# Kernel tuning notes

Measured on AMD Instinct MI355X. Metric: run time of the kernel, lower is better.

Reference implementation:

```python
import jax, jax.numpy as jnp
import numpy as np

N = 100000          # nodes
E = 1600000         # edges (avg degree 16)
D = 128             # prototype feature dim
C = 100             # num classes
NUM_LAYERS = 3      # propagation layers


def setup_inputs() -> dict:
    key = jax.random.key(0)
    k1, k2, k3, k4 = jax.random.split(key, 4)
    train_mask = jax.random.randint(k1, (N,), 0, 2) > 0                # bool [N]
    labels_all = jax.random.randint(k2, (N,), 0, C)                    # int   [N]
    edge_index = jax.random.randint(k3, (2, E), 0, N)                  # int   [2,E]
    global_protos = jax.random.normal(k4, (C, D), dtype=jnp.float32)   # [C,D]
    alpha = jnp.float32(0.5)                                           # learnable scalar
    return dict(train_mask=train_mask, global_protos=global_protos,
                labels_all=labels_all, edge_index=edge_index, alpha=alpha)


def _label_propagate(y0, edge_index, alpha):
    # symmetric GCN normalization D^-1/2 A D^-1/2 (no self loops), as in PyG LabelPropagation
    src, dst = edge_index[0], edge_index[1]
    deg = jax.ops.segment_sum(jnp.ones((E,), y0.dtype), dst, num_segments=N)
    deg_inv_sqrt = jnp.where(deg > 0, jax.lax.rsqrt(jnp.maximum(deg, 1.0)), 0.0)
    norm = deg_inv_sqrt[src] * deg_inv_sqrt[dst]                       # [E]
    res = (1.0 - alpha) * y0                                           # residual term
    out = y0
    for _ in range(NUM_LAYERS):
        msgs = out[src] * norm[:, None]                                # gather [E,D]
        agg = jax.ops.segment_sum(msgs, dst, num_segments=N)           # scatter-add [N,D]
        out = jnp.clip(alpha * agg + res, 0.0, 1.0)                    # post_step clamp
    return out


def reference(train_mask, global_protos, labels_all, edge_index, alpha):
    # proto_rep[train_mask] = global_protos[labels_all[train_mask]], zeros elsewhere
    y0 = jnp.where(train_mask[:, None], global_protos[labels_all], 0.0)  # [N,D]
    return _label_propagate(y0, edge_index, alpha)
```

## Files before the change

### kernel.cpp

```cpp
#include <hip/hip_runtime.h>
#include <stdint.h>

typedef _Float16 f16;

#define N_NODES 100000
#define N_EDGES 1600000
#define CAP     64
#define NC      196
#define SLOTS   40
#define SEGCAP  12288
#define EPB     4096
#define SPAD    (CAP + 4)


__global__ __launch_bounds__(256) void bin_kernel(
    const int* __restrict__ src, const int* __restrict__ dst,
    int* __restrict__ gcur, unsigned int* __restrict__ gbins) {
    __shared__ int lcnt[NC];
    __shared__ int gb[NC];
    __shared__ unsigned int lbuf[NC * SLOTS];
    int t = threadIdx.x;
    for (int b = t; b < NC; b += 256) lcnt[b] = 0;
    __syncthreads();

    int base = blockIdx.x * EPB;
    int sv[16], dv[16];
#pragma unroll
    for (int k = 0; k < 16; ++k) {
        int i = base + k * 256 + t;
        sv[k] = (i < N_EDGES) ? src[i] : -1;
        dv[k] = (i < N_EDGES) ? dst[i] : 0;
    }
#pragma unroll
    for (int k = 0; k < 16; ++k) {
        if (sv[k] >= 0) {
            int d = dv[k];
            int cb = d >> 9;
            unsigned rec = (unsigned)sv[k] | ((unsigned)(d & 511) << 17);
            int pos = atomicAdd(&lcnt[cb], 1);
            if (pos < SLOTS) {
                lbuf[cb * SLOTS + pos] = rec;
            } else {
                int gp = atomicAdd(&gcur[cb], 1);
                if (gp < SEGCAP) gbins[(size_t)cb * SEGCAP + gp] = rec;
            }
        }
    }
    __syncthreads();
    if (t < NC) {
        int c = lcnt[t]; if (c > SLOTS) c = SLOTS;
        gb[t] = atomicAdd(&gcur[t], c);
    }
    __syncthreads();
    int wave = t >> 6, lane = t & 63;
    for (int b = wave; b < NC; b += 4) {
        int c = lcnt[b]; if (c > SLOTS) c = SLOTS;
        if (lane < c)
            gbins[(size_t)b * SEGCAP + gb[b] + lane] = lbuf[b * SLOTS + lane];
    }
}


__global__ __launch_bounds__(512) void csr_kernel(
    const unsigned int* __restrict__ gbins, const int* __restrict__ gcur,
    int* __restrict__ cnt, int* __restrict__ csr, float* __restrict__ dis,
    const int* __restrict__ mask, const int* __restrict__ labels,
    int* __restrict__ c0, int2* __restrict__ meta,
    const float* __restrict__ protos, f16* __restrict__ pf16) {
    __shared__ int lc[128];
    __shared__ int rows[128][CAP];
    int cb = blockIdx.x >> 2;
    int sb = blockIdx.x & 3;
    int t = threadIdx.x;
    if (t < 128) lc[t] = 0;
    __syncthreads();
    int m = gcur[cb]; if (m > SEGCAP) m = SEGCAP;
    const unsigned int* seg = gbins + (size_t)cb * SEGCAP;
    int base = (cb << 9) + (sb << 7);
    for (int i = t; i < m; i += 512) {
        unsigned v = seg[i];
        int dl = (int)(v >> 17);
        if ((dl >> 7) == sb) {
            int local = dl & 127;
            int pos = atomicAdd(&lc[local], 1);
            if (pos < CAP) rows[local][pos] = (int)(v & 0x1FFFF);
        }
    }
    __syncthreads();
    if (t < 128) {
        int n = base + t;
        if (n < N_NODES) {
            int d = lc[t];
            cnt[n] = d;
            float dv = (d > 0) ? rsqrtf((float)d) : 0.0f;
            dis[n] = dv;
            int c = mask[n] ? labels[n] : -1;
            c0[n] = c;
            meta[n] = make_int2(__float_as_int(dv), c);
        }
    }
    uint4* csr4 = (uint4*)csr;
    for (int idx = t; idx < 128 * 16; idx += 512) {
        int node = idx >> 4, ch = idx & 15;
        int n = base + node;
        if (n < N_NODES) {
            int d = lc[node]; if (d > CAP) d = CAP;
            if (ch * 4 < d) {
                uint4 w;
                w.x = (unsigned)rows[node][ch * 4 + 0];
                w.y = (unsigned)rows[node][ch * 4 + 1];
                w.z = (unsigned)rows[node][ch * 4 + 2];
                w.w = (unsigned)rows[node][ch * 4 + 3];
                csr4[(size_t)n * 16 + ch] = w;
            }
        }
    }
    if (blockIdx.x < 25) pf16[blockIdx.x * 512 + t] = (f16)protos[blockIdx.x * 512 + t];
}


__global__ __launch_bounds__(256) void prop0_kernel(
    const f16* __restrict__ pf16, uint8_t* __restrict__ out,
    const int* __restrict__ cnt, const int* __restrict__ csr,
    const float* __restrict__ dis, const int* __restrict__ c0,
    const int2* __restrict__ meta, int2* __restrict__ csr2,
    const float* __restrict__ protos, const float* __restrict__ alpha_p) {
    __shared__ uint2 smeta[4][4][SPAD];
    int t = threadIdx.x;
    int wave = t >> 6, lane = t & 63;
    int grp = lane >> 4, s16 = lane & 15;
    int n = blockIdx.x * 16 + wave * 4 + grp;

    float alpha = *alpha_p;
    int m = cnt[n]; if (m > CAP) m = CAP;
    float dn = dis[n];
    const int* bucket = csr + (size_t)n * CAP;
    int2* bucket2 = csr2 + (size_t)n * CAP;

    int mm = m;
    { int o = __shfl_xor(mm, 16); mm = mm > o ? mm : o;
      o = __shfl_xor(mm, 32);     mm = mm > o ? mm : o; }
    int mp = (mm + 3) & ~3;

    for (int e = s16; e < mp; e += 16) {
        unsigned wb = 0, off = 0;
        if (e < m) {
            int s = bucket[e];
            int2 mt = meta[s];
            float wpre = __int_as_float(mt.x) * dn;
            bucket2[e] = make_int2(s, __float_as_int(wpre));
            int c = mt.y;
            if (c >= 0) { wb = __float_as_uint(wpre); off = (unsigned)c << 4; }
        }
        smeta[wave][grp][e] = make_uint2(wb, off);
    }

    const uint4* md = (const uint4*)&smeta[wave][grp][0];
    const uint4* r4 = (const uint4*)pf16;
    float acc[8] = {0.f, 0.f, 0.f, 0.f, 0.f, 0.f, 0.f, 0.f};

    uint4 mA0, mA1, gA0, gA1, gA2, gA3;
    uint4 mB0, mB1, gB0, gB1, gB2, gB3;
#define LOADB(MM0, MM1, G0, G1, G2, G3, J) do {            \
    MM0 = md[(J) >> 1]; MM1 = md[((J) >> 1) + 1];          \
    G0 = r4[MM0.y + s16]; G1 = r4[MM0.w + s16];            \
    G2 = r4[MM1.y + s16]; G3 = r4[MM1.w + s16]; } while (0)
#define COMP1(WB, G) do {                                  \
    union { uint4 u; f16 h[8]; } q_; q_.u = (G);           \
    float w_ = __uint_as_float(WB);                        \
    _Pragma("unroll")                                      \
    for (int i_ = 0; i_ < 8; ++i_)                         \
        acc[i_] = fmaf((float)q_.h[i_], w_, acc[i_]); } while (0)
#define COMP(MM0, MM1, G0, G1, G2, G3) do {                \
    COMP1(MM0.x, G0); COMP1(MM0.z, G1);                    \
    COMP1(MM1.x, G2); COMP1(MM1.z, G3); } while (0)
    if (mp > 0) {
        LOADB(mA0, mA1, gA0, gA1, gA2, gA3, 0);
        for (int j = 0; j < mp; j += 8) {
            if (j + 4 < mp) LOADB(mB0, mB1, gB0, gB1, gB2, gB3, j + 4);
            COMP(mA0, mA1, gA0, gA1, gA2, gA3);
            if (j + 8 < mp) LOADB(mA0, mA1, gA0, gA1, gA2, gA3, j + 8);
            if (j + 4 < mp) COMP(mB0, mB1, gB0, gB1, gB2, gB3);
        }
    }
#undef LOADB
#undef COMP1
#undef COMP

    int cn = c0[n];
    float ra = 1.f - alpha;
    float y[8] = {0.f, 0.f, 0.f, 0.f, 0.f, 0.f, 0.f, 0.f};
    if (cn >= 0) {
        const float4* pr = (const float4*)(protos + (size_t)cn * 128) + (s16 << 1);
        float4 p0 = pr[0], p1 = pr[1];
        y[0] = p0.x; y[1] = p0.y; y[2] = p0.z; y[3] = p0.w;
        y[4] = p1.x; y[5] = p1.y; y[6] = p1.z; y[7] = p1.w;
    }
    unsigned q[8];
#pragma unroll
    for (int i = 0; i < 8; ++i) {
        float o = fminf(fmaxf(fmaf(alpha, acc[i], ra * y[i]), 0.f), 1.f);
        q[i] = (unsigned)(o * 255.f + 0.5f);
    }
    unsigned lo = q[0] | (q[1] << 8) | (q[2] << 16) | (q[3] << 24);
    unsigned hi = q[4] | (q[5] << 8) | (q[6] << 16) | (q[7] << 24);
    ((uint2*)out)[((size_t)n << 4) + s16] = make_uint2(lo, hi);
}


template <int MODE>
__global__ __launch_bounds__(256) void prop_kernel(
    const uint8_t* __restrict__ rows_, void* __restrict__ out,
    const int* __restrict__ cnt, const int2* __restrict__ csr2,
    const int* __restrict__ c0,
    const float* __restrict__ protos, const float* __restrict__ alpha_p) {
    __shared__ uint2 smeta[4][4][SPAD];
    int t = threadIdx.x;
    int wave = t >> 6, lane = t & 63;
    int grp = lane >> 4, s16 = lane & 15;
    int n = blockIdx.x * 16 + wave * 4 + grp;

    float alpha = *alpha_p;
    int m = cnt[n]; if (m > CAP) m = CAP;
    const int2* bucket2 = csr2 + (size_t)n * CAP;
    const float inv255 = 1.0f / 255.0f;

    int mm = m;
    { int o = __shfl_xor(mm, 16); mm = mm > o ? mm : o;
      o = __shfl_xor(mm, 32);     mm = mm > o ? mm : o; }
    int mp = (mm + 3) & ~3;

    for (int e = s16; e < mp; e += 16) {
        unsigned wb = 0, off = 0;
        if (e < m) {
            int2 rec = bucket2[e];
            off = (unsigned)rec.x << 4;
            wb = __float_as_uint(__int_as_float(rec.y) * inv255);
        }
        smeta[wave][grp][e] = make_uint2(wb, off);
    }

    const uint4* md = (const uint4*)&smeta[wave][grp][0];
    const uint2* r2 = (const uint2*)rows_;
    float acc[8] = {0.f, 0.f, 0.f, 0.f, 0.f, 0.f, 0.f, 0.f};

    uint4 mA0, mA1, mB0, mB1;
    uint2 gA0, gA1, gA2, gA3, gB0, gB1, gB2, gB3;
#define LOADB(MM0, MM1, G0, G1, G2, G3, J) do {            \
    MM0 = md[(J) >> 1]; MM1 = md[((J) >> 1) + 1];          \
    G0 = r2[MM0.y + s16]; G1 = r2[MM0.w + s16];            \
    G2 = r2[MM1.y + s16]; G3 = r2[MM1.w + s16]; } while (0)
#define COMP1(WB, G) do {                                  \
    float w_ = __uint_as_float(WB);                        \
    unsigned x_ = (G).x, y_ = (G).y;                       \
    acc[0] = fmaf((float)(x_ & 0xffu),         w_, acc[0]); \
    acc[1] = fmaf((float)((x_ >> 8) & 0xffu),  w_, acc[1]); \
    acc[2] = fmaf((float)((x_ >> 16) & 0xffu), w_, acc[2]); \
    acc[3] = fmaf((float)(x_ >> 24),           w_, acc[3]); \
    acc[4] = fmaf((float)(y_ & 0xffu),         w_, acc[4]); \
    acc[5] = fmaf((float)((y_ >> 8) & 0xffu),  w_, acc[5]); \
    acc[6] = fmaf((float)((y_ >> 16) & 0xffu), w_, acc[6]); \
    acc[7] = fmaf((float)(y_ >> 24),           w_, acc[7]); } while (0)
#define COMP(MM0, MM1, G0, G1, G2, G3) do {                \
    COMP1(MM0.x, G0); COMP1(MM0.z, G1);                    \
    COMP1(MM1.x, G2); COMP1(MM1.z, G3); } while (0)
    if (mp > 0) {
        LOADB(mA0, mA1, gA0, gA1, gA2, gA3, 0);
        for (int j = 0; j < mp; j += 8) {
            if (j + 4 < mp) LOADB(mB0, mB1, gB0, gB1, gB2, gB3, j + 4);
            COMP(mA0, mA1, gA0, gA1, gA2, gA3);
            if (j + 8 < mp) LOADB(mA0, mA1, gA0, gA1, gA2, gA3, j + 8);
            if (j + 4 < mp) COMP(mB0, mB1, gB0, gB1, gB2, gB3);
        }
    }
#undef LOADB
#undef COMP1
#undef COMP

    int cn = c0[n];
    float ra = 1.f - alpha;
    float y[8] = {0.f, 0.f, 0.f, 0.f, 0.f, 0.f, 0.f, 0.f};
    if (cn >= 0) {
        const float4* pr = (const float4*)(protos + (size_t)cn * 128) + (s16 << 1);
        float4 p0 = pr[0], p1 = pr[1];
        y[0] = p0.x; y[1] = p0.y; y[2] = p0.z; y[3] = p0.w;
        y[4] = p1.x; y[5] = p1.y; y[6] = p1.z; y[7] = p1.w;
    }
    float o[8];
#pragma unroll
    for (int i = 0; i < 8; ++i)
        o[i] = fminf(fmaxf(fmaf(alpha, acc[i], ra * y[i]), 0.f), 1.f);

    if (MODE == 2) {
        float4* dst = (float4*)out + ((size_t)n << 5) + (s16 << 1);
        dst[0] = make_float4(o[0], o[1], o[2], o[3]);
        dst[1] = make_float4(o[4], o[5], o[6], o[7]);
    } else {
        unsigned q[8];
#pragma unroll
        for (int i = 0; i < 8; ++i) q[i] = (unsigned)(o[i] * 255.f + 0.5f);
        unsigned lo = q[0] | (q[1] << 8) | (q[2] << 16) | (q[3] << 24);
        unsigned hi = q[4] | (q[5] << 8) | (q[6] << 16) | (q[7] << 24);
        ((uint2*)out)[((size_t)n << 4) + s16] = make_uint2(lo, hi);
    }
}


extern "C" void kernel_launch(void* const* d_in, const int* in_sizes, int n_in,
                              void* d_out, int out_size, void* d_ws, size_t ws_size,
                              hipStream_t stream) {
    const int*   mask   = (const int*)d_in[0];
    const float* protos = (const float*)d_in[1];
    const int*   labels = (const int*)d_in[2];
    const int*   ei     = (const int*)d_in[3];
    const float* alpha  = (const float*)d_in[4];
    const int* src = ei;
    const int* dst = ei + N_EDGES;

    int*          gcur  = (int*)d_ws;
    int*          cnt   = gcur + 256;
    float*        dis   = (float*)(cnt + N_NODES);
    int*          c0    = (int*)(dis + N_NODES);
    int2*         meta  = (int2*)(c0 + N_NODES);
    int*          csr   = (int*)(meta + N_NODES);
    int2*         csr2  = (int2*)(csr + (size_t)N_NODES * CAP);
    f16*          pf16  = (f16*)(csr2 + (size_t)N_NODES * CAP);
    unsigned char* region = (unsigned char*)(pf16 + 16384);
    unsigned int* gbins = (unsigned int*)region;
    uint8_t*      bufA  = (uint8_t*)region;
    uint8_t*      bufB  = bufA + (size_t)N_NODES * 128;

    hipMemsetAsync(gcur, 0, 256 * sizeof(int), stream);

    int bgrid = (N_EDGES + EPB - 1) / EPB;
    bin_kernel<<<bgrid, 256, 0, stream>>>(src, dst, gcur, gbins);
    csr_kernel<<<NC * 4, 512, 0, stream>>>(gbins, gcur, cnt, csr, dis,
                                           mask, labels, c0, meta, protos, pf16);

    int pgrid = N_NODES / 16;
    prop0_kernel<<<pgrid, 256, 0, stream>>>(pf16, bufA, cnt, csr, dis, c0,
                                            meta, csr2, protos, alpha);
    prop_kernel<1><<<pgrid, 256, 0, stream>>>(bufA, bufB, cnt, csr2, c0,
                                              protos, alpha);
    prop_kernel<2><<<pgrid, 256, 0, stream>>>(bufB, d_out, cnt, csr2, c0,
                                              protos, alpha);
}
```

Measured before the change: 218.9 us.

## Move edge metadata enrichment into separate kernel and deepen prop gather pipeline

Adds an enrich_kernel that builds csr2 records for all edges, packing the source id and the source's class+1 into one word alongside the precomputed normalized weight. prop0 then reads these records instead of doing the dependent csr→meta gather and writing csr2 itself. Separately, prop_kernel now prefetches 8 neighbor rows per batch instead of 4 (mp padded to 8), giving more loads in flight. The cost is an extra kernel launch, a full pass over csr, more registers in prop_kernel, and the assumption that node ids fit in 17 bits. Enrich reads dn from meta[n].x, where the old code used dis[n], which may not match.

```diff
diff --git a/kernel.cpp b/kernel.cpp
--- a/kernel.cpp
+++ b/kernel.cpp
@@ -119,11 +119,31 @@
 }
 
 
+__global__ __launch_bounds__(256) void enrich_kernel(
+    const int* __restrict__ csr, const int* __restrict__ cnt,
+    const int2* __restrict__ meta, int2* __restrict__ csr2) {
+    int tid = blockIdx.x * 256 + threadIdx.x;
+    const int total = N_NODES * CAP;
+    const int stride = 3125 * 256;
+    for (int i = tid; i < total; i += stride) {
+        int n = i >> 6, e = i & 63;
+        int d = cnt[n];
+        if (e < d) {
+            int s = csr[i];
+            int2 mt = meta[s];
+            float dn = __int_as_float(meta[n].x);
+            float wpre = __int_as_float(mt.x) * dn;
+            unsigned pack = (unsigned)s | ((unsigned)(mt.y + 1) << 17);
+            csr2[i] = make_int2((int)pack, __float_as_int(wpre));
+        }
+    }
+}
+
+
 __global__ __launch_bounds__(256) void prop0_kernel(
     const f16* __restrict__ pf16, uint8_t* __restrict__ out,
-    const int* __restrict__ cnt, const int* __restrict__ csr,
-    const float* __restrict__ dis, const int* __restrict__ c0,
-    const int2* __restrict__ meta, int2* __restrict__ csr2,
+    const int* __restrict__ cnt, const int2* __restrict__ csr2,
+    const int* __restrict__ c0,
     const float* __restrict__ protos, const float* __restrict__ alpha_p) {
     __shared__ uint2 smeta[4][4][SPAD];
     int t = threadIdx.x;
@@ -133,9 +153,7 @@
 
     float alpha = *alpha_p;
     int m = cnt[n]; if (m > CAP) m = CAP;
-    float dn = dis[n];
-    const int* bucket = csr + (size_t)n * CAP;
-    int2* bucket2 = csr2 + (size_t)n * CAP;
+    const int2* bucket2 = csr2 + (size_t)n * CAP;
 
     int mm = m;
     { int o = __shfl_xor(mm, 16); mm = mm > o ? mm : o;
@@ -145,12 +163,12 @@
     for (int e = s16; e < mp; e += 16) {
         unsigned wb = 0, off = 0;
         if (e < m) {
-            int s = bucket[e];
-            int2 mt = meta[s];
-            float wpre = __int_as_float(mt.x) * dn;
-            bucket2[e] = make_int2(s, __float_as_int(wpre));
-            int c = mt.y;
-            if (c >= 0) { wb = __float_as_uint(wpre); off = (unsigned)c << 4; }
+            int2 rec = bucket2[e];
+            unsigned cp1 = (unsigned)rec.x >> 17;
+            if (cp1 > 0) {
+                wb = (unsigned)rec.y;
+                off = (cp1 - 1) << 4;
+            }
         }
         smeta[wave][grp][e] = make_uint2(wb, off);
     }
@@ -228,13 +246,13 @@
     int mm = m;
     { int o = __shfl_xor(mm, 16); mm = mm > o ? mm : o;
       o = __shfl_xor(mm, 32);     mm = mm > o ? mm : o; }
-    int mp = (mm + 3) & ~3;
+    int mp = (mm + 7) & ~7;
 
     for (int e = s16; e < mp; e += 16) {
         unsigned wb = 0, off = 0;
         if (e < m) {
             int2 rec = bucket2[e];
-            off = (unsigned)rec.x << 4;
+            off = ((unsigned)rec.x & 0x1FFFFu) << 4;
             wb = __float_as_uint(__int_as_float(rec.y) * inv255);
         }
         smeta[wave][grp][e] = make_uint2(wb, off);
@@ -244,12 +262,15 @@
     const uint2* r2 = (const uint2*)rows_;
     float acc[8] = {0.f, 0.f, 0.f, 0.f, 0.f, 0.f, 0.f, 0.f};
 
-    uint4 mA0, mA1, mB0, mB1;
-    uint2 gA0, gA1, gA2, gA3, gB0, gB1, gB2, gB3;
-#define LOADB(MM0, MM1, G0, G1, G2, G3, J) do {            \
-    MM0 = md[(J) >> 1]; MM1 = md[((J) >> 1) + 1];          \
-    G0 = r2[MM0.y + s16]; G1 = r2[MM0.w + s16];            \
-    G2 = r2[MM1.y + s16]; G3 = r2[MM1.w + s16]; } while (0)
+    uint4 mA[4], mB[4];
+    uint2 gA[8], gB[8];
+#define LOADB8(MM, G, J) do {                              \
+    MM[0] = md[(J) >> 1];       MM[1] = md[((J) >> 1) + 1];\
+    MM[2] = md[((J) >> 1) + 2]; MM[3] = md[((J) >> 1) + 3];\
+    G[0] = r2[MM[0].y + s16]; G[1] = r2[MM[0].w + s16];    \
+    G[2] = r2[MM[1].y + s16]; G[3] = r2[MM[1].w + s16];    \
+    G[4] = r2[MM[2].y + s16]; G[5] = r2[MM[2].w + s16];    \
+    G[6] = r2[MM[3].y + s16]; G[7] = r2[MM[3].w + s16]; } while (0)
 #define COMP1(WB, G) do {                                  \
     float w_ = __uint_as_float(WB);                        \
     unsigned x_ = (G).x, y_ = (G).y;                       \
@@ -261,21 +282,23 @@
     acc[5] = fmaf((float)((y_ >> 8) & 0xffu),  w_, acc[5]); \
     acc[6] = fmaf((float)((y_ >> 16) & 0xffu), w_, acc[6]); \
     acc[7] = fmaf((float)(y_ >> 24),           w_, acc[7]); } while (0)
-#define COMP(MM0, MM1, G0, G1, G2, G3) do {                \
-    COMP1(MM0.x, G0); COMP1(MM0.z, G1);                    \
-    COMP1(MM1.x, G2); COMP1(MM1.z, G3); } while (0)
+#define COMP8(MM, G) do {                                  \
+    COMP1(MM[0].x, G[0]); COMP1(MM[0].z, G[1]);            \
+    COMP1(MM[1].x, G[2]); COMP1(MM[1].z, G[3]);            \
+    COMP1(MM[2].x, G[4]); COMP1(MM[2].z, G[5]);            \
+    COMP1(MM[3].x, G[6]); COMP1(MM[3].z, G[7]); } while (0)
     if (mp > 0) {
-        LOADB(mA0, mA1, gA0, gA1, gA2, gA3, 0);
-        for (int j = 0; j < mp; j += 8) {
-            if (j + 4 < mp) LOADB(mB0, mB1, gB0, gB1, gB2, gB3, j + 4);
-            COMP(mA0, mA1, gA0, gA1, gA2, gA3);
-            if (j + 8 < mp) LOADB(mA0, mA1, gA0, gA1, gA2, gA3, j + 8);
-            if (j + 4 < mp) COMP(mB0, mB1, gB0, gB1, gB2, gB3);
-        }
-    }
-#undef LOADB
+        LOADB8(mA, gA, 0);
+        for (int j = 0; j < mp; j += 16) {
+            if (j + 8 < mp) LOADB8(mB, gB, j + 8);
+            COMP8(mA, gA);
+            if (j + 16 < mp) LOADB8(mA, gA, j + 16);
+            if (j + 8 < mp) COMP8(mB, gB);
+        }
+    }
+#undef LOADB8
 #undef COMP1
-#undef COMP
+#undef COMP8
 
     int cn = c0[n];
     float ra = 1.f - alpha;
@@ -336,10 +359,11 @@
     bin_kernel<<<bgrid, 256, 0, stream>>>(src, dst, gcur, gbins);
     csr_kernel<<<NC * 4, 512, 0, stream>>>(gbins, gcur, cnt, csr, dis,
                                            mask, labels, c0, meta, protos, pf16);
+    enrich_kernel<<<3125, 256, 0, stream>>>(csr, cnt, meta, csr2);
 
     int pgrid = N_NODES / 16;
-    prop0_kernel<<<pgrid, 256, 0, stream>>>(pf16, bufA, cnt, csr, dis, c0,
-                                            meta, csr2, protos, alpha);
+    prop0_kernel<<<pgrid, 256, 0, stream>>>(pf16, bufA, cnt, csr2, c0,
+                                            protos, alpha);
     prop_kernel<1><<<pgrid, 256, 0, stream>>>(bufA, bufB, cnt, csr2, c0,
                                               protos, alpha);
     prop_kernel<2><<<pgrid, 256, 0, stream>>>(bufB, d_out, cnt, csr2, c0,
```

New measurement: 234.2 us. +7.0%, slower.
